# Kernel tuning notes

Measured on AMD Instinct MI355X. Metric: run time of the kernel, lower is better.

## Reference

```python
import jax, jax.numpy as jnp
import numpy as np

N = 100000      # nodes
E = 1600000     # edges (avg degree 16)
F_IN = 128      # node feature dim
HID = 128       # conv1 out
EMB = 64        # conv2 out (embedding)
OUT = 40        # classes


def setup_inputs() -> dict:
    key = jax.random.key(0)
    ks = jax.random.split(key, 8)
    x = jax.random.normal(ks[0], (N, F_IN), dtype=jnp.float32)
    edge_index = jax.random.randint(ks[1], (2, E), 0, N, dtype=jnp.int64)

    def glorot(k, shape):
        lim = np.sqrt(6.0 / (shape[0] + shape[1])).astype(np.float32)
        return jax.random.uniform(k, shape, jnp.float32, -lim, lim)

    W1 = glorot(ks[2], (F_IN, HID)); b1 = jnp.zeros((HID,), jnp.float32)
    W2 = glorot(ks[3], (HID, EMB)); b2 = jnp.zeros((EMB,), jnp.float32)
    Wl = glorot(ks[4], (EMB, OUT)); bl = jnp.zeros((OUT,), jnp.float32)
    return {"x": x, "edge_index": edge_index,
            "W1": W1, "b1": b1, "W2": W2, "b2": b2, "Wl": Wl, "bl": bl}


def _gcn_conv(x, W, b, src, dst, norm, n):
    # GCNConv: linear transform first (smaller width earlier), then normalized
    # sparse aggregation: out_i = sum_{j->i} norm_e * (x_j W) + b
    h = x @ W
    out = jax.ops.segment_sum(h[src] * norm[:, None], dst, num_segments=n)
    return out + b


def reference(x, edge_index, W1, b1, W2, b2, Wl, bl):
    n = x.shape[0]
    loop = jnp.arange(n, dtype=edge_index.dtype)
    # add self loops (GCNConv default)
    src = jnp.concatenate([edge_index[0], loop])
    dst = jnp.concatenate([edge_index[1], loop])
    # symmetric degree normalization: D^{-1/2} (A+I) D^{-1/2}
    deg = jax.ops.segment_sum(jnp.ones_like(dst, x.dtype), dst, num_segments=n)
    dinv = jnp.where(deg > 0, jax.lax.rsqrt(deg), 0.0)
    norm = dinv[src] * dinv[dst]

    h = jax.nn.relu(_gcn_conv(x, W1, b1, src, dst, norm, n))
    # F.dropout(training=False) is identity in eval mode
    embedding = _gcn_conv(h, W2, b2, src, dst, norm, n)
    logits = embedding @ Wl + bl
    return jax.nn.log_softmax(logits, axis=1), embedding
```

## Files before the change

kernel.cpp:

```cpp
#include <hip/hip_runtime.h>
#include <math.h>

#define F_IN 128
#define HIDN 128
#define EMBD 64
#define OUTC 40

#define NBINS 1024
#define BIN_SHIFT 7
#define CSR_BLKS 256

__host__ __device__ static inline int imin(int a, int b) { return a < b ? a : b; }

typedef __attribute__((ext_vector_type(8))) short s16x8;
typedef __attribute__((ext_vector_type(4))) float f32x4;

__device__ __forceinline__ unsigned short f2bf(float f) {
    unsigned int u = __builtin_bit_cast(unsigned int, f);
    u = (u + 0x7FFFu + ((u >> 16) & 1u)) >> 16;
    return (unsigned short)u;
}
__device__ __forceinline__ float bflo(unsigned int v) {
    return __builtin_bit_cast(float, v << 16);
}
__device__ __forceinline__ float bfhi(unsigned int v) {
    return __builtin_bit_cast(float, v & 0xFFFF0000u);
}


__global__ __launch_bounds__(256) void coarse_hist_kernel(const int* __restrict__ dst,
                                                          int* __restrict__ bc, int E) {
    __shared__ int h[NBINS];
    for (int i = threadIdx.x; i < NBINS; i += 256) h[i] = 0;
    __syncthreads();
    const int chunk = (E + CSR_BLKS - 1) / CSR_BLKS;
    const int e0 = blockIdx.x * chunk;
    const int e1 = imin(e0 + chunk, E);
    for (int e = e0 + threadIdx.x; e < e1; e += 256)
        atomicAdd(&h[dst[e] >> BIN_SHIFT], 1);
    __syncthreads();
    for (int i = threadIdx.x; i < NBINS; i += 256)
        bc[blockIdx.x * NBINS + i] = h[i];
}

__global__ __launch_bounds__(1024) void bin_base_kernel(int* __restrict__ bc,
                                                        int* __restrict__ cs) {
    __shared__ int s[NBINS];
    const int t = threadIdx.x;
    int run = 0;
    for (int blk = 0; blk < CSR_BLKS; ++blk) {
        int v = bc[blk * NBINS + t];
        bc[blk * NBINS + t] = run;
        run += v;
    }
    s[t] = run;
    __syncthreads();
    for (int off = 1; off < NBINS; off <<= 1) {
        int v = (t >= off) ? s[t - off] : 0;
        __syncthreads();
        s[t] += v;
        __syncthreads();
    }
    cs[t + 1] = s[t];
    if (t == 0) cs[0] = 0;
}

__global__ __launch_bounds__(256) void bin_scatter_kernel(const int* __restrict__ src,
                                                          const int* __restrict__ dst,
                                                          const int* __restrict__ bc,
                                                          const int* __restrict__ cs,
                                                          int* __restrict__ ebuf, int E) {
    __shared__ int cur[NBINS];
    for (int i = threadIdx.x; i < NBINS; i += 256)
        cur[i] = cs[i] + bc[blockIdx.x * NBINS + i];
    __syncthreads();
    const int chunk = (E + CSR_BLKS - 1) / CSR_BLKS;
    const int e0 = blockIdx.x * chunk;
    const int e1 = imin(e0 + chunk, E);
    for (int e = e0 + threadIdx.x; e < e1; e += 256) {
        int d = dst[e];
        int pos = atomicAdd(&cur[d >> BIN_SHIFT], 1);
        ebuf[pos] = (src[e] << BIN_SHIFT) | (d & 127);
    }
}

__global__ __launch_bounds__(256) void fine_build_kernel(const int* __restrict__ ebuf,
                                                         const int* __restrict__ cs,
                                                         int* __restrict__ degi,
                                                         int* __restrict__ rowptr,
                                                         float* __restrict__ dinv,
                                                         int* __restrict__ col, int n) {
    __shared__ int h[128];
    __shared__ int fs[128];
    __shared__ int cur[128];
    const int b = blockIdx.x;
    const int node0 = b << BIN_SHIFT;
    const int t = threadIdx.x;
    if (t < 128) h[t] = 0;
    __syncthreads();
    const int e0 = cs[b], e1 = cs[b + 1];
    for (int e = e0 + t; e < e1; e += 256)
        atomicAdd(&h[ebuf[e] & 127], 1);
    __syncthreads();
    if (t < 128) fs[t] = h[t];
    __syncthreads();
    for (int off = 1; off < 128; off <<= 1) {
        int v = 0;
        if (t < 128 && t >= off) v = fs[t - off];
        __syncthreads();
        if (t < 128) fs[t] += v;
        __syncthreads();
    }
    if (t < 128) {
        int node = node0 + t;
        if (node < n) {
            int cnt = h[t];
            degi[node] = cnt;
            rowptr[node] = e0 + fs[t] - cnt;
            dinv[node] = rsqrtf((float)cnt + 1.0f);
        }
        cur[t] = 0;
    }
    __syncthreads();
    for (int e = e0 + t; e < e1; e += 256) {
        int p = ebuf[e];
        int li = p & 127;
        int loc = atomicAdd(&cur[li], 1);
        col[e0 + (fs[li] - h[li]) + loc] = p >> BIN_SHIFT;
    }
}

template <typename InT, int K, int M, int WM, int WN>
__global__ __launch_bounds__(256) void gemm_mfma_kernel(const InT* __restrict__ X,
                                                        const float* __restrict__ W,
                                                        const float* __restrict__ dinv,
                                                        unsigned short* __restrict__ Y,
                                                        int n, int ntiles) {
    constexpr int BM = 64;
    constexpr int WR = BM / WM;
    constexpr int WC = M / WN;
    constexpr int RF = WR / 16;
    constexpr int CF = WC / 16;
    constexpr int KS = K / 32;
    constexpr int ROWB = K * 2;
    constexpr int UPR = ROWB / 16;

    __shared__ char Xs[BM * ROWB];

    const int tid = threadIdx.x;
    const int lane = tid & 63;
    const int wid = tid >> 6;
    const int wrow = wid / WN;
    const int wcol = wid % WN;
    const int l15 = lane & 15;
    const int lhi = lane >> 4;

    s16x8 bfrag[CF][KS];
#pragma unroll
    for (int cf = 0; cf < CF; ++cf)
#pragma unroll
        for (int ks = 0; ks < KS; ++ks) {
            const int colg = wcol * WC + cf * 16 + l15;
            const int kbase = ks * 32 + lhi * 8;
            s16x8 b;
#pragma unroll
            for (int j = 0; j < 8; ++j)
                b[j] = (short)f2bf(W[(size_t)(kbase + j) * M + colg]);
            bfrag[cf][ks] = b;
        }

    for (int tile = blockIdx.x; tile < ntiles; tile += gridDim.x) {
        const int row0 = tile * BM;
        __syncthreads();
#pragma unroll
        for (int i = 0; i < (BM * UPR) / 256; ++i) {
            int g = i * 256 + tid;
            int r = g / UPR, u = g % UPR;
            int grow = row0 + r;
            int4 val = make_int4(0, 0, 0, 0);
            if (grow < n) {
                if constexpr (sizeof(InT) == 4) {
                    const float* src = (const float*)X + (size_t)grow * K + u * 8;
                    float4 f0 = *(const float4*)src;
                    float4 f1 = *(const float4*)(src + 4);
                    val.x = (int)(f2bf(f0.x) | ((unsigned int)f2bf(f0.y) << 16));
                    val.y = (int)(f2bf(f0.z) | ((unsigned int)f2bf(f0.w) << 16));
                    val.z = (int)(f2bf(f1.x) | ((unsigned int)f2bf(f1.y) << 16));
                    val.w = (int)(f2bf(f1.z) | ((unsigned int)f2bf(f1.w) << 16));
                } else {
                    val = *(const int4*)((const unsigned short*)X + (size_t)grow * K + u * 8);
                }
            }
            *(int4*)(Xs + r * ROWB + ((u ^ (r & 7)) * 16)) = val;
        }
        __syncthreads();

        f32x4 acc[RF][CF];
#pragma unroll
        for (int rf = 0; rf < RF; ++rf)
#pragma unroll
            for (int cf = 0; cf < CF; ++cf) acc[rf][cf] = (f32x4)(0.0f);
#pragma unroll
        for (int ks = 0; ks < KS; ++ks) {
            s16x8 afrag[RF];
#pragma unroll
            for (int rf = 0; rf < RF; ++rf) {
                int r = wrow * WR + rf * 16 + l15;
                int u = ks * 4 + lhi;
                afrag[rf] = *(const s16x8*)(Xs + r * ROWB + ((u ^ (r & 7)) * 16));
            }
#pragma unroll
            for (int rf = 0; rf < RF; ++rf)
#pragma unroll
                for (int cf = 0; cf < CF; ++cf)
                    acc[rf][cf] = __builtin_amdgcn_mfma_f32_16x16x32_bf16(
                        afrag[rf], bfrag[cf][ks], acc[rf][cf], 0, 0, 0);
        }

#pragma unroll
        for (int rf = 0; rf < RF; ++rf) {
#pragma unroll
            for (int reg = 0; reg < 4; ++reg) {
                int grow = row0 + wrow * WR + rf * 16 + lhi * 4 + reg;
                if (grow < n) {
                    float dv = dinv[grow];
#pragma unroll
                    for (int cf = 0; cf < CF; ++cf) {
                        int colg = wcol * WC + cf * 16 + l15;
                        Y[(size_t)grow * M + colg] = f2bf(acc[rf][cf][reg] * dv);
                    }
                }
            }
        }
    }
}

__global__ __launch_bounds__(256) void gather_gemm_kernel(
    const unsigned short* __restrict__ Hs1, const int* __restrict__ rowptr,
    const int* __restrict__ degi, const int* __restrict__ col,
    const float* __restrict__ dinv, const float* __restrict__ b1,
    const float* __restrict__ W2, unsigned short* __restrict__ Hs2, int n) {
    __shared__ char h_tile[16 * 256];

    const int tid = threadIdx.x;
    const int lane = tid & 63;
    const int wv = tid >> 6;
    const int sub = lane & 15;
    const int grp = lane >> 4;
    const int node0 = blockIdx.x * 16;
    const int local = wv * 4 + grp;
    const int node = node0 + local;
    const int foff = sub * 8;

    s16x8 bfrag[4];
#pragma unroll
    for (int ks = 0; ks < 4; ++ks) {
        const int colg = wv * 16 + sub;
        const int kbase = ks * 32 + grp * 8;
        s16x8 bb;
#pragma unroll
        for (int j = 0; j < 8; ++j)
            bb[j] = (short)f2bf(W2[(size_t)(kbase + j) * EMBD + colg]);
        bfrag[ks] = bb;
    }

    if (node < n) {
        const int start = rowptr[node];
        const int cnt = degi[node];
        const float dvn = dinv[node];
        float acc[8];
        {
            int4 v = *(const int4*)(Hs1 + (size_t)node * HIDN + foff);
#pragma unroll
            for (int q = 0; q < 4; ++q) {
                unsigned int w = ((const unsigned int*)&v)[q];
                acc[2 * q] = bflo(w);
                acc[2 * q + 1] = bfhi(w);
            }
        }
        int m0 = imin(cnt, 16);
        int sv = (sub < m0) ? col[start + sub] : 0;
        for (int base = 0; base < cnt; base += 16) {
            int m = imin(cnt - base, 16);
            int svn = 0;
            int nb = base + 16;
            if (nb < cnt) {
                int mn = imin(cnt - nb, 16);
                svn = (sub < mn) ? col[start + nb + sub] : 0;
            }
            int k = 0;
            for (; k + 8 <= m; k += 8) {
                int4 a[8];
#pragma unroll
                for (int j = 0; j < 8; ++j) {
                    int s = __shfl(sv, k + j, 16);
                    a[j] = *(const int4*)(Hs1 + (size_t)s * HIDN + foff);
                }
#pragma unroll
                for (int j = 0; j < 8; ++j)
#pragma unroll
                    for (int q = 0; q < 4; ++q) {
                        unsigned int w = ((const unsigned int*)&a[j])[q];
                        acc[2 * q] += bflo(w);
                        acc[2 * q + 1] += bfhi(w);
                    }
            }
            for (; k + 2 <= m; k += 2) {
                int s0 = __shfl(sv, k, 16);
                int s1 = __shfl(sv, k + 1, 16);
                int4 a0 = *(const int4*)(Hs1 + (size_t)s0 * HIDN + foff);
                int4 a1 = *(const int4*)(Hs1 + (size_t)s1 * HIDN + foff);
#pragma unroll
                for (int q = 0; q < 4; ++q) {
                    unsigned int w0 = ((const unsigned int*)&a0)[q];
                    unsigned int w1 = ((const unsigned int*)&a1)[q];
                    acc[2 * q] += bflo(w0);
                    acc[2 * q + 1] += bfhi(w0);
                    acc[2 * q] += bflo(w1);
                    acc[2 * q + 1] += bfhi(w1);
                }
            }
            for (; k < m; ++k) {
                int s = __shfl(sv, k, 16);
                int4 a = *(const int4*)(Hs1 + (size_t)s * HIDN + foff);
#pragma unroll
                for (int q = 0; q < 4; ++q) {
                    unsigned int w = ((const unsigned int*)&a)[q];
                    acc[2 * q] += bflo(w);
                    acc[2 * q + 1] += bfhi(w);
                }
            }
            sv = svn;
        }
        float4 bv0 = *(const float4*)(b1 + foff);
        float4 bv1 = *(const float4*)(b1 + foff + 4);
        float o[8];
        o[0] = fmaxf(dvn * acc[0] + bv0.x, 0.f);
        o[1] = fmaxf(dvn * acc[1] + bv0.y, 0.f);
        o[2] = fmaxf(dvn * acc[2] + bv0.z, 0.f);
        o[3] = fmaxf(dvn * acc[3] + bv0.w, 0.f);
        o[4] = fmaxf(dvn * acc[4] + bv1.x, 0.f);
        o[5] = fmaxf(dvn * acc[5] + bv1.y, 0.f);
        o[6] = fmaxf(dvn * acc[6] + bv1.z, 0.f);
        o[7] = fmaxf(dvn * acc[7] + bv1.w, 0.f);
        int4 p;
        ((unsigned int*)&p)[0] = f2bf(o[0]) | ((unsigned int)f2bf(o[1]) << 16);
        ((unsigned int*)&p)[1] = f2bf(o[2]) | ((unsigned int)f2bf(o[3]) << 16);
        ((unsigned int*)&p)[2] = f2bf(o[4]) | ((unsigned int)f2bf(o[5]) << 16);
        ((unsigned int*)&p)[3] = f2bf(o[6]) | ((unsigned int)f2bf(o[7]) << 16);
        *(int4*)(h_tile + local * 256 + ((sub ^ (local & 7)) * 16)) = p;
    }
    __syncthreads();

    f32x4 acc2 = (f32x4)(0.0f);
#pragma unroll
    for (int ks = 0; ks < 4; ++ks) {
        int r = sub;
        int u = ks * 4 + grp;
        s16x8 af = *(const s16x8*)(h_tile + r * 256 + ((u ^ (r & 7)) * 16));
        acc2 = __builtin_amdgcn_mfma_f32_16x16x32_bf16(af, bfrag[ks], acc2, 0, 0, 0);
    }
#pragma unroll
    for (int reg = 0; reg < 4; ++reg) {
        int row = grp * 4 + reg;
        int nd = node0 + row;
        if (nd < n)
            Hs2[(size_t)nd * EMBD + wv * 16 + sub] = f2bf(acc2[reg] * dinv[nd]);
    }
}

template <int F, bool RELU, bool OBF>
__global__ __launch_bounds__(256) void gather_kernel(const unsigned short* __restrict__ Hs,
                                                     const int* __restrict__ rowptr,
                                                     const int* __restrict__ degi,
                                                     const int* __restrict__ col,
                                                     const float* __restrict__ dinv,
                                                     const float* __restrict__ b,
                                                     float* __restrict__ outf,
                                                     unsigned short* __restrict__ outb,
                                                     int n) {
    constexpr int LPF = F / 8;
    constexpr int NPW = 64 / LPF;
    const int lane = threadIdx.x & 63;
    const int wv = threadIdx.x >> 6;
    const int sub = lane & (LPF - 1);
    const int grp = lane / LPF;
    const int node = (blockIdx.x * 4 + wv) * NPW + grp;
    if (node >= n) return;
    const int start = rowptr[node];
    const int cnt = degi[node];
    const int foff = sub * 8;
    const float dvn = dinv[node];

    float acc[8];
    {
        int4 v = *(const int4*)(Hs + (size_t)node * F + foff);
#pragma unroll
        for (int q = 0; q < 4; ++q) {
            unsigned int w = ((const unsigned int*)&v)[q];
            acc[2 * q] = bflo(w);
            acc[2 * q + 1] = bfhi(w);
        }
    }

    int m0 = imin(cnt, LPF);
    int sv = (sub < m0) ? col[start + sub] : 0;
    for (int base = 0; base < cnt; base += LPF) {
        int m = imin(cnt - base, LPF);
        int svn = 0;
        int nb = base + LPF;
        if (nb < cnt) {
            int mn = imin(cnt - nb, LPF);
            svn = (sub < mn) ? col[start + nb + sub] : 0;
        }
        int k = 0;
        for (; k + 8 <= m; k += 8) {
            int4 a[8];
#pragma unroll
            for (int j = 0; j < 8; ++j) {
                int s = __shfl(sv, k + j, LPF);
                a[j] = *(const int4*)(Hs + (size_t)s * F + foff);
            }
#pragma unroll
            for (int j = 0; j < 8; ++j)
#pragma unroll
                for (int q = 0; q < 4; ++q) {
                    unsigned int w = ((const unsigned int*)&a[j])[q];
                    acc[2 * q] += bflo(w);
                    acc[2 * q + 1] += bfhi(w);
                }
        }
        for (; k + 2 <= m; k += 2) {
            int s0 = __shfl(sv, k, LPF);
            int s1 = __shfl(sv, k + 1, LPF);
            int4 a0 = *(const int4*)(Hs + (size_t)s0 * F + foff);
            int4 a1 = *(const int4*)(Hs + (size_t)s1 * F + foff);
#pragma unroll
            for (int q = 0; q < 4; ++q) {
                unsigned int w0 = ((const unsigned int*)&a0)[q];
                unsigned int w1 = ((const unsigned int*)&a1)[q];
                acc[2 * q] += bflo(w0);
                acc[2 * q + 1] += bfhi(w0);
                acc[2 * q] += bflo(w1);
                acc[2 * q + 1] += bfhi(w1);
            }
        }
        for (; k < m; ++k) {
            int s = __shfl(sv, k, LPF);
            int4 a = *(const int4*)(Hs + (size_t)s * F + foff);
#pragma unroll
            for (int q = 0; q < 4; ++q) {
                unsigned int w = ((const unsigned int*)&a)[q];
                acc[2 * q] += bflo(w);
                acc[2 * q + 1] += bfhi(w);
            }
        }
        sv = svn;
    }

    float4 bv0 = *(const float4*)(b + foff);
    float4 bv1 = *(const float4*)(b + foff + 4);
    float o[8];
    o[0] = dvn * acc[0] + bv0.x; o[1] = dvn * acc[1] + bv0.y;
    o[2] = dvn * acc[2] + bv0.z; o[3] = dvn * acc[3] + bv0.w;
    o[4] = dvn * acc[4] + bv1.x; o[5] = dvn * acc[5] + bv1.y;
    o[6] = dvn * acc[6] + bv1.z; o[7] = dvn * acc[7] + bv1.w;
    if (RELU) {
#pragma unroll
        for (int j = 0; j < 8; ++j) o[j] = fmaxf(o[j], 0.0f);
    }
    if constexpr (OBF) {
        int4 p;
        ((unsigned int*)&p)[0] = f2bf(o[0]) | ((unsigned int)f2bf(o[1]) << 16);
        ((unsigned int*)&p)[1] = f2bf(o[2]) | ((unsigned int)f2bf(o[3]) << 16);
        ((unsigned int*)&p)[2] = f2bf(o[4]) | ((unsigned int)f2bf(o[5]) << 16);
        ((unsigned int*)&p)[3] = f2bf(o[6]) | ((unsigned int)f2bf(o[7]) << 16);
        *(int4*)(outb + (size_t)node * F + foff) = p;
    } else {
        float4 w0 = make_float4(o[0], o[1], o[2], o[3]);
        float4 w1 = make_float4(o[4], o[5], o[6], o[7]);
        *(float4*)(outf + (size_t)node * F + foff) = w0;
        *(float4*)(outf + (size_t)node * F + foff + 4) = w1;
    }
}

#define LSM_STRIDE 257
__global__ __launch_bounds__(256) void logits_lsm_kernel(const float* __restrict__ emb,
                                                         const float* __restrict__ Wl,
                                                         const float* __restrict__ bl,
                                                         float* __restrict__ out, int n) {
    __shared__ float Sbuf[EMBD * LSM_STRIDE];
    __shared__ float Wls[EMBD * OUTC];
    __shared__ float bls[OUTC];
    const int tid = threadIdx.x;
    const int node0 = blockIdx.x * 256;
    for (int i = tid; i < EMBD * OUTC; i += 256) Wls[i] = Wl[i];
    if (tid < OUTC) bls[tid] = bl[tid];

    const size_t base = (size_t)node0 * EMBD;
    const size_t total_elems = (size_t)n * EMBD;
    for (int it = 0; it < 16; ++it) {
        int idx = (tid + it * 256) * 4;
        int r = idx / EMBD, f = idx % EMBD;
        float4 v = make_float4(0.f, 0.f, 0.f, 0.f);
        if (base + idx + 3 < total_elems) v = *(const float4*)(emb + base + idx);
        Sbuf[(f + 0) * LSM_STRIDE + r] = v.x;
        Sbuf[(f + 1) * LSM_STRIDE + r] = v.y;
        Sbuf[(f + 2) * LSM_STRIDE + r] = v.z;
        Sbuf[(f + 3) * LSM_STRIDE + r] = v.w;
    }
    __syncthreads();

    float logit[OUTC];
#pragma unroll
    for (int o = 0; o < OUTC; ++o) logit[o] = bls[o];
    for (int f = 0; f < EMBD; ++f) {
        float ef = Sbuf[f * LSM_STRIDE + tid];
#pragma unroll
        for (int o = 0; o < OUTC; ++o) logit[o] = fmaf(ef, Wls[f * OUTC + o], logit[o]);
    }
    float mx = -INFINITY;
#pragma unroll
    for (int o = 0; o < OUTC; ++o) mx = fmaxf(mx, logit[o]);
    float s = 0.0f;
#pragma unroll
    for (int o = 0; o < OUTC; ++o) s += expf(logit[o] - mx);
    float lse = mx + logf(s);
    __syncthreads();
#pragma unroll
    for (int o = 0; o < OUTC; ++o) Sbuf[o * LSM_STRIDE + tid] = logit[o] - lse;
    __syncthreads();

    const size_t obase = (size_t)node0 * OUTC;
    const size_t ototal = (size_t)n * OUTC;
    for (int idx = tid; idx < 256 * OUTC; idx += 256) {
        size_t g = obase + idx;
        if (g < ototal) out[g] = Sbuf[(idx % OUTC) * LSM_STRIDE + (idx / OUTC)];
    }
}

extern "C" void kernel_launch(void* const* d_in, const int* in_sizes, int n_in,
                              void* d_out, int out_size, void* d_ws, size_t ws_size,
                              hipStream_t stream) {
    const float* x  = (const float*)d_in[0];
    const int*   ei = (const int*)d_in[1];
    const float* W1 = (const float*)d_in[2];
    const float* b1 = (const float*)d_in[3];
    const float* W2 = (const float*)d_in[4];
    const float* b2 = (const float*)d_in[5];
    const float* Wl = (const float*)d_in[6];
    const float* bl = (const float*)d_in[7];

    const int N = in_sizes[0] / F_IN;
    const int E = in_sizes[1] / 2;
    const int* srcp = ei;
    const int* dstp = ei + E;

    float* out = (float*)d_out;
    float* lsm = out;
    float* emb = out + (size_t)N * OUTC;

    float* ws    = (float*)d_ws;
    float* dinv  = ws;
    int*   degi  = (int*)(ws + N);
    int*   rowptr= degi + N;
    int*   cs    = rowptr + N;
    int*   bc    = cs + 1056;
    int*   col   = bc + CSR_BLKS * NBINS;
    int*   ebuf  = col + E;
    unsigned short* Hs1 = (unsigned short*)(ebuf + E);
    unsigned short* Hs2 = Hs1 + (size_t)N * HIDN;

    const int B = 256;
    const int ntiles = (N + 63) / 64;

    coarse_hist_kernel<<<CSR_BLKS, B, 0, stream>>>(dstp, bc, E);
    bin_base_kernel<<<1, 1024, 0, stream>>>(bc, cs);
    bin_scatter_kernel<<<CSR_BLKS, B, 0, stream>>>(srcp, dstp, bc, cs, ebuf, E);
    fine_build_kernel<<<(N + 127) / 128, B, 0, stream>>>(ebuf, cs, degi, rowptr, dinv, col, N);

    gemm_mfma_kernel<float, F_IN, HIDN, 2, 2><<<784, B, 0, stream>>>(x, W1, dinv, Hs1, N, ntiles);

    gather_gemm_kernel<<<(N + 15) / 16, B, 0, stream>>>(
        Hs1, rowptr, degi, col, dinv, b1, W2, Hs2, N);

    gather_kernel<EMBD, false, false><<<(N + 31) / 32, B, 0, stream>>>(
        Hs2, rowptr, degi, col, dinv, b2, emb, nullptr, N);

    logits_lsm_kernel<<<(N + 255) / 256, B, 0, stream>>>(emb, Wl, bl, lsm, N);
}
```

Measured before the change: 230.3 us.

## Fuse second-layer gather with logits and log-softmax epilogue

Merges the layer-2 aggregation kernel and the separate logits/log-softmax kernel into one kernel. Each 8-lane group computes partial logits from its 8 embedding features against Wl held in shared memory, then reduces them with a recursive-halving shuffle so each lane ends up owning 5 classes. The log-softmax is done with group shuffles, and results are staged in shared memory for coalesced output. This removes one launch and the re-read of the fp32 embedding, at the cost of more registers (40 partials) and shuffle work inside the gather kernel.

```diff
diff --git a/kernel.cpp b/kernel.cpp
--- a/kernel.cpp
+++ b/kernel.cpp
@@ -369,173 +369,163 @@
     }
 }
 
-template <int F, bool RELU, bool OBF>
-__global__ __launch_bounds__(256) void gather_kernel(const unsigned short* __restrict__ Hs,
-                                                     const int* __restrict__ rowptr,
-                                                     const int* __restrict__ degi,
-                                                     const int* __restrict__ col,
-                                                     const float* __restrict__ dinv,
-                                                     const float* __restrict__ b,
-                                                     float* __restrict__ outf,
-                                                     unsigned short* __restrict__ outb,
-                                                     int n) {
-    constexpr int LPF = F / 8;
-    constexpr int NPW = 64 / LPF;
-    const int lane = threadIdx.x & 63;
-    const int wv = threadIdx.x >> 6;
-    const int sub = lane & (LPF - 1);
-    const int grp = lane / LPF;
-    const int node = (blockIdx.x * 4 + wv) * NPW + grp;
-    if (node >= n) return;
-    const int start = rowptr[node];
-    const int cnt = degi[node];
+__global__ __launch_bounds__(256) void gather_logits_kernel(
+    const unsigned short* __restrict__ Hs, const int* __restrict__ rowptr,
+    const int* __restrict__ degi, const int* __restrict__ col,
+    const float* __restrict__ dinv, const float* __restrict__ b2,
+    const float* __restrict__ Wl, const float* __restrict__ bl,
+    float* __restrict__ emb, float* __restrict__ lsm, int n) {
+    __shared__ float Wls[EMBD * 41];
+    __shared__ float bls[OUTC];
+    __shared__ float stage[4][8 * OUTC];
+
+    const int tid = threadIdx.x;
+    for (int i = tid; i < EMBD * OUTC; i += 256)
+        Wls[(i / OUTC) * 41 + (i % OUTC)] = Wl[i];
+    if (tid < OUTC) bls[tid] = bl[tid];
+    __syncthreads();
+
+    const int lane = tid & 63;
+    const int wv = tid >> 6;
+    const int sub = lane & 7;
+    const int grp = lane >> 3;
+    const int wbase = (blockIdx.x * 4 + wv) * 8;
+    const int node = wbase + grp;
     const int foff = sub * 8;
-    const float dvn = dinv[node];
-
-    float acc[8];
-    {
-        int4 v = *(const int4*)(Hs + (size_t)node * F + foff);
-#pragma unroll
-        for (int q = 0; q < 4; ++q) {
-            unsigned int w = ((const unsigned int*)&v)[q];
-            acc[2 * q] = bflo(w);
-            acc[2 * q + 1] = bfhi(w);
-        }
-    }
-
-    int m0 = imin(cnt, LPF);
-    int sv = (sub < m0) ? col[start + sub] : 0;
-    for (int base = 0; base < cnt; base += LPF) {
-        int m = imin(cnt - base, LPF);
-        int svn = 0;
-        int nb = base + LPF;
-        if (nb < cnt) {
-            int mn = imin(cnt - nb, LPF);
-            svn = (sub < mn) ? col[start + nb + sub] : 0;
-        }
-        int k = 0;
-        for (; k + 8 <= m; k += 8) {
-            int4 a[8];
-#pragma unroll
-            for (int j = 0; j < 8; ++j) {
-                int s = __shfl(sv, k + j, LPF);
-                a[j] = *(const int4*)(Hs + (size_t)s * F + foff);
-            }
-#pragma unroll
-            for (int j = 0; j < 8; ++j)
+
+    if (node < n) {
+        const int start = rowptr[node];
+        const int cnt = degi[node];
+        const float dvn = dinv[node];
+
+        float acc[8];
+        {
+            int4 v = *(const int4*)(Hs + (size_t)node * EMBD + foff);
+#pragma unroll
+            for (int q = 0; q < 4; ++q) {
+                unsigned int w = ((const unsigned int*)&v)[q];
+                acc[2 * q] = bflo(w);
+                acc[2 * q + 1] = bfhi(w);
+            }
+        }
+        int m0 = imin(cnt, 8);
+        int sv = (sub < m0) ? col[start + sub] : 0;
+        for (int base = 0; base < cnt; base += 8) {
+            int m = imin(cnt - base, 8);
+            int svn = 0;
+            int nb = base + 8;
+            if (nb < cnt) {
+                int mn = imin(cnt - nb, 8);
+                svn = (sub < mn) ? col[start + nb + sub] : 0;
+            }
+            int k = 0;
+            for (; k + 8 <= m; k += 8) {
+                int4 a[8];
+#pragma unroll
+                for (int j = 0; j < 8; ++j) {
+                    int s = __shfl(sv, k + j, 8);
+                    a[j] = *(const int4*)(Hs + (size_t)s * EMBD + foff);
+                }
+#pragma unroll
+                for (int j = 0; j < 8; ++j)
+#pragma unroll
+                    for (int q = 0; q < 4; ++q) {
+                        unsigned int w = ((const unsigned int*)&a[j])[q];
+                        acc[2 * q] += bflo(w);
+                        acc[2 * q + 1] += bfhi(w);
+                    }
+            }
+            for (; k < m; ++k) {
+                int s = __shfl(sv, k, 8);
+                int4 a = *(const int4*)(Hs + (size_t)s * EMBD + foff);
 #pragma unroll
                 for (int q = 0; q < 4; ++q) {
-                    unsigned int w = ((const unsigned int*)&a[j])[q];
+                    unsigned int w = ((const unsigned int*)&a)[q];
                     acc[2 * q] += bflo(w);
                     acc[2 * q + 1] += bfhi(w);
                 }
-        }
-        for (; k + 2 <= m; k += 2) {
-            int s0 = __shfl(sv, k, LPF);
-            int s1 = __shfl(sv, k + 1, LPF);
-            int4 a0 = *(const int4*)(Hs + (size_t)s0 * F + foff);
-            int4 a1 = *(const int4*)(Hs + (size_t)s1 * F + foff);
-#pragma unroll
-            for (int q = 0; q < 4; ++q) {
-                unsigned int w0 = ((const unsigned int*)&a0)[q];
-                unsigned int w1 = ((const unsigned int*)&a1)[q];
-                acc[2 * q] += bflo(w0);
-                acc[2 * q + 1] += bfhi(w0);
-                acc[2 * q] += bflo(w1);
-                acc[2 * q + 1] += bfhi(w1);
-            }
-        }
-        for (; k < m; ++k) {
-            int s = __shfl(sv, k, LPF);
-            int4 a = *(const int4*)(Hs + (size_t)s * F + foff);
-#pragma unroll
-            for (int q = 0; q < 4; ++q) {
-                unsigned int w = ((const unsigned int*)&a)[q];
-                acc[2 * q] += bflo(w);
-                acc[2 * q + 1] += bfhi(w);
-            }
-        }
-        sv = svn;
-    }
-
-    float4 bv0 = *(const float4*)(b + foff);
-    float4 bv1 = *(const float4*)(b + foff + 4);
-    float o[8];
-    o[0] = dvn * acc[0] + bv0.x; o[1] = dvn * acc[1] + bv0.y;
-    o[2] = dvn * acc[2] + bv0.z; o[3] = dvn * acc[3] + bv0.w;
-    o[4] = dvn * acc[4] + bv1.x; o[5] = dvn * acc[5] + bv1.y;
-    o[6] = dvn * acc[6] + bv1.z; o[7] = dvn * acc[7] + bv1.w;
-    if (RELU) {
-#pragma unroll
-        for (int j = 0; j < 8; ++j) o[j] = fmaxf(o[j], 0.0f);
-    }
-    if constexpr (OBF) {
-        int4 p;
-        ((unsigned int*)&p)[0] = f2bf(o[0]) | ((unsigned int)f2bf(o[1]) << 16);
-        ((unsigned int*)&p)[1] = f2bf(o[2]) | ((unsigned int)f2bf(o[3]) << 16);
-        ((unsigned int*)&p)[2] = f2bf(o[4]) | ((unsigned int)f2bf(o[5]) << 16);
-        ((unsigned int*)&p)[3] = f2bf(o[6]) | ((unsigned int)f2bf(o[7]) << 16);
-        *(int4*)(outb + (size_t)node * F + foff) = p;
-    } else {
-        float4 w0 = make_float4(o[0], o[1], o[2], o[3]);
-        float4 w1 = make_float4(o[4], o[5], o[6], o[7]);
-        *(float4*)(outf + (size_t)node * F + foff) = w0;
-        *(float4*)(outf + (size_t)node * F + foff + 4) = w1;
-    }
-}
-
-#define LSM_STRIDE 257
-__global__ __launch_bounds__(256) void logits_lsm_kernel(const float* __restrict__ emb,
-                                                         const float* __restrict__ Wl,
-                                                         const float* __restrict__ bl,
-                                                         float* __restrict__ out, int n) {
-    __shared__ float Sbuf[EMBD * LSM_STRIDE];
-    __shared__ float Wls[EMBD * OUTC];
-    __shared__ float bls[OUTC];
-    const int tid = threadIdx.x;
-    const int node0 = blockIdx.x * 256;
-    for (int i = tid; i < EMBD * OUTC; i += 256) Wls[i] = Wl[i];
-    if (tid < OUTC) bls[tid] = bl[tid];
-
-    const size_t base = (size_t)node0 * EMBD;
-    const size_t total_elems = (size_t)n * EMBD;
-    for (int it = 0; it < 16; ++it) {
-        int idx = (tid + it * 256) * 4;
-        int r = idx / EMBD, f = idx % EMBD;
-        float4 v = make_float4(0.f, 0.f, 0.f, 0.f);
-        if (base + idx + 3 < total_elems) v = *(const float4*)(emb + base + idx);
-        Sbuf[(f + 0) * LSM_STRIDE + r] = v.x;
-        Sbuf[(f + 1) * LSM_STRIDE + r] = v.y;
-        Sbuf[(f + 2) * LSM_STRIDE + r] = v.z;
-        Sbuf[(f + 3) * LSM_STRIDE + r] = v.w;
-    }
-    __syncthreads();
-
-    float logit[OUTC];
-#pragma unroll
-    for (int o = 0; o < OUTC; ++o) logit[o] = bls[o];
-    for (int f = 0; f < EMBD; ++f) {
-        float ef = Sbuf[f * LSM_STRIDE + tid];
-#pragma unroll
-        for (int o = 0; o < OUTC; ++o) logit[o] = fmaf(ef, Wls[f * OUTC + o], logit[o]);
-    }
-    float mx = -INFINITY;
-#pragma unroll
-    for (int o = 0; o < OUTC; ++o) mx = fmaxf(mx, logit[o]);
-    float s = 0.0f;
-#pragma unroll
-    for (int o = 0; o < OUTC; ++o) s += expf(logit[o] - mx);
-    float lse = mx + logf(s);
-    __syncthreads();
-#pragma unroll
-    for (int o = 0; o < OUTC; ++o) Sbuf[o * LSM_STRIDE + tid] = logit[o] - lse;
-    __syncthreads();
-
-    const size_t obase = (size_t)node0 * OUTC;
-    const size_t ototal = (size_t)n * OUTC;
-    for (int idx = tid; idx < 256 * OUTC; idx += 256) {
-        size_t g = obase + idx;
-        if (g < ototal) out[g] = Sbuf[(idx % OUTC) * LSM_STRIDE + (idx / OUTC)];
+            }
+            sv = svn;
+        }
+
+        float4 bv0 = *(const float4*)(b2 + foff);
+        float4 bv1 = *(const float4*)(b2 + foff + 4);
+        float o[8];
+        o[0] = dvn * acc[0] + bv0.x; o[1] = dvn * acc[1] + bv0.y;
+        o[2] = dvn * acc[2] + bv0.z; o[3] = dvn * acc[3] + bv0.w;
+        o[4] = dvn * acc[4] + bv1.x; o[5] = dvn * acc[5] + bv1.y;
+        o[6] = dvn * acc[6] + bv1.z; o[7] = dvn * acc[7] + bv1.w;
+        *(float4*)(emb + (size_t)node * EMBD + foff) = make_float4(o[0], o[1], o[2], o[3]);
+        *(float4*)(emb + (size_t)node * EMBD + foff + 4) = make_float4(o[4], o[5], o[6], o[7]);
+
+        float partial[OUTC];
+#pragma unroll
+        for (int oc = 0; oc < OUTC; ++oc) partial[oc] = 0.0f;
+#pragma unroll
+        for (int j = 0; j < 8; ++j) {
+            float ef = o[j];
+            const float* wrow = &Wls[(foff + j) * 41];
+#pragma unroll
+            for (int oc = 0; oc < OUTC; ++oc)
+                partial[oc] = fmaf(ef, wrow[oc], partial[oc]);
+        }
+        const bool q0 = (sub & 1) != 0;
+        float a1[20];
+#pragma unroll
+        for (int j = 0; j < 20; ++j) {
+            float give = q0 ? partial[j] : partial[20 + j];
+            float recv = __shfl_xor(give, 1, 8);
+            float keep = q0 ? partial[20 + j] : partial[j];
+            a1[j] = keep + recv;
+        }
+        const bool q1 = (sub & 2) != 0;
+        float a2[10];
+#pragma unroll
+        for (int j = 0; j < 10; ++j) {
+            float give = q1 ? a1[j] : a1[10 + j];
+            float recv = __shfl_xor(give, 2, 8);
+            float keep = q1 ? a1[10 + j] : a1[j];
+            a2[j] = keep + recv;
+        }
+        const bool q2 = (sub & 4) != 0;
+        float c[5];
+#pragma unroll
+        for (int j = 0; j < 5; ++j) {
+            float give = q2 ? a2[j] : a2[5 + j];
+            float recv = __shfl_xor(give, 4, 8);
+            float keep = q2 ? a2[5 + j] : a2[j];
+            c[j] = keep + recv;
+        }
+        const int ocb = (sub & 1) * 20 + ((sub >> 1) & 1) * 10 + ((sub >> 2) & 1) * 5;
+#pragma unroll
+        for (int j = 0; j < 5; ++j) c[j] += bls[ocb + j];
+        float mx = c[0];
+#pragma unroll
+        for (int j = 1; j < 5; ++j) mx = fmaxf(mx, c[j]);
+#pragma unroll
+        for (int mask = 1; mask < 8; mask <<= 1) mx = fmaxf(mx, __shfl_xor(mx, mask, 8));
+        float ss = 0.0f;
+#pragma unroll
+        for (int j = 0; j < 5; ++j) ss += expf(c[j] - mx);
+#pragma unroll
+        for (int mask = 1; mask < 8; mask <<= 1) ss += __shfl_xor(ss, mask, 8);
+        float lse = mx + logf(ss);
+#pragma unroll
+        for (int j = 0; j < 5; ++j) stage[wv][grp * OUTC + ocb + j] = c[j] - lse;
+    }
+    __syncthreads();
+
+    {
+        int valid = n - wbase;
+        if (valid > 8) valid = 8;
+        if (valid > 0) {
+#pragma unroll
+            for (int j = 0; j < 5; ++j) {
+                int idx = lane * 5 + j;
+                if (idx < valid * OUTC)
+                    lsm[(size_t)wbase * OUTC + idx] = stage[wv][idx];
+            }
+        }
     }
 }
 
@@ -584,8 +574,6 @@
     gather_gemm_kernel<<<(N + 15) / 16, B, 0, stream>>>(
         Hs1, rowptr, degi, col, dinv, b1, W2, Hs2, N);
 
-    gather_kernel<EMBD, false, false><<<(N + 31) / 32, B, 0, stream>>>(
-        Hs2, rowptr, degi, col, dinv, b2, emb, nullptr, N);
-
-    logits_lsm_kernel<<<(N + 255) / 256, B, 0, stream>>>(emb, Wl, bl, lsm, N);
-}
+    gather_logits_kernel<<<(N + 31) / 32, B, 0, stream>>>(
+        Hs2, rowptr, degi, col, dinv, b2, Wl, bl, emb, lsm, N);
+}
```

Measured after the change: 234.9 us. No clear change (+2.0%).
